# Kernel optimization log

Measured on AMD Instinct MI355X. Metric: run time of the kernel, lower is better.

The kernel has to match this reference:

```python
import jax, jax.numpy as jnp
import numpy as np

N, E, K = 20000, 320000, 4
IN, HID, OUT, HD = 512, 256, 128, 256


def setup_inputs() -> dict:
    key = jax.random.key(0)
    ks = jax.random.split(key, 12)
    def lin(k, fi, fo):
        return jax.random.normal(k, (fi, fo), jnp.float32) / np.sqrt(fi)
    return {
        "x": jax.random.normal(ks[0], (N, IN), jnp.float32),
        "edge_index": jax.random.randint(ks[1], (K, 2, E), 0, N),
        "value": jax.random.normal(ks[2], (K, 3), jnp.float32),
        "index": jax.random.randint(ks[3], (K, 2), 0, N),
        "W1": lin(ks[4], IN, HID),  "b1": jnp.zeros((HID,), jnp.float32),
        "W2": lin(ks[5], HID, OUT), "b2": jnp.zeros((OUT,), jnp.float32),
        "Wd": lin(ks[6], 2 * OUT + 3, HD), "bd": jnp.zeros((HD,), jnp.float32),
        "Wp": lin(ks[7], HD, 1),    "bp": jnp.zeros((1,), jnp.float32),
    }


def reference(x, edge_index, value, index, W1, b1, W2, b2, Wd, bd, Wp, bp):
    n = x.shape[0]
    loops = jnp.arange(n)

    def gcn(h, src, dst, W, b):
        # GCNConv: symmetric normalization with self-loops already in src/dst
        deg = jnp.zeros((n,), h.dtype).at[dst].add(1.0)
        dinv = jnp.where(deg > 0, deg ** -0.5, 0.0)
        norm = dinv[src] * dinv[dst]                      # [E+N]
        msg = (h @ W)[src] * norm[:, None]                # [E+N, F_out]
        return jnp.zeros((n, W.shape[1]), h.dtype).at[dst].add(msg) + b

    def encode(ei):
        src = jnp.concatenate([ei[0], loops])             # add self-loops
        dst = jnp.concatenate([ei[1], loops])
        h = jax.nn.relu(gcn(x, src, dst, W1, b1))
        return gcn(h, src, dst, W2, b2)                   # [N, OUT]

    def step(carry, inp):
        ei, val, idx = inp
        mu = encode(ei)
        h = jnp.concatenate([mu[idx[0]], mu[idx[1]], val])  # [2*OUT+3]
        o = jax.nn.relu(h @ Wd + bd)
        p = jax.nn.sigmoid(o @ Wp + bp)
        return carry, p[0]

    _, preds = jax.lax.scan(step, None, (edge_index, value, index))
    return preds  # [K]
```

## Files before the change

kernel.cpp:

```cpp
#include <hip/hip_runtime.h>
#include <hip/hip_bf16.h>

#define NN 20000
#define EE 320000
#define E4 (EE/4)
#define KK 4
#define FIN 512
#define FHID 256
#define FOUT 128
#define FHD 256
#define NH (2*FOUT+3)
#define CAP1 1024
#define MS2 128
#define BCAP 256

__device__ __forceinline__ float dinvf(int indeg) {
  return rsqrtf((float)(indeg + 1));
}

__global__ __launch_bounds__(256) void kz_zero(int4* __restrict__ p, int n4) {
  int i = blockIdx.x * 256 + threadIdx.x;
  if (i < n4) p[i] = make_int4(0, 0, 0, 0);
}

__global__ __launch_bounds__(256) void k12_scan_claim(const int* __restrict__ ei,
                                                      const int* __restrict__ idx,
                                                      int* __restrict__ cnt1,
                                                      int* __restrict__ L1src,
                                                      int* __restrict__ L1sel,
                                                      int* __restrict__ reg,
                                                      int* __restrict__ slotNode,
                                                      int* __restrict__ mslots) {
  int k = blockIdx.y;
  int* rk = reg + (size_t)k * NN;
  int t0 = idx[2 * k], t1 = idx[2 * k + 1];
  if (blockIdx.x == 0 && threadIdx.x < 2) {
    int node = (threadIdx.x == 0) ? t0 : t1;
    if (atomicCAS(&rk[node], 0, -2) == 0) {
      int s = atomicAdd(&mslots[k], 1);
      if (s < MS2) { slotNode[k * MS2 + s] = node; rk[node] = s + 1; }
    }
  }
  int e4 = blockIdx.x * blockDim.x + threadIdx.x;
  if (e4 >= E4) return;
  const int* srcp = ei + (size_t)k * 2 * EE;
  int4 d4 = ((const int4*)(srcp + EE))[e4];
  int ds[4] = {d4.x, d4.y, d4.z, d4.w};
  #pragma unroll
  for (int c = 0; c < 4; c++) {
    bool h0 = (ds[c] == t0), h1 = (ds[c] == t1);
    if (h0 || h1) {
      int u = srcp[e4 * 4 + c];
      if (h0) {
        int p = atomicAdd(&cnt1[k], 1);
        if (p < CAP1) { L1src[k * CAP1 + p] = u; L1sel[k * CAP1 + p] = 0; }
      }
      if (h1) {
        int p = atomicAdd(&cnt1[k], 1);
        if (p < CAP1) { L1src[k * CAP1 + p] = u; L1sel[k * CAP1 + p] = 1; }
      }
      if (atomicCAS(&rk[u], 0, -2) == 0) {
        int s = atomicAdd(&mslots[k], 1);
        if (s < MS2) { slotNode[k * MS2 + s] = u; rk[u] = s + 1; }
      }
    }
  }
}

__global__ __launch_bounds__(256) void k3_scanL2(const int* __restrict__ ei,
                                                 int* __restrict__ reg,
                                                 int* __restrict__ bcnt,
                                                 int* __restrict__ bucket) {
  int k = blockIdx.y;
  int e4 = blockIdx.x * blockDim.x + threadIdx.x;
  if (e4 >= E4) return;
  const int* srcp = ei + (size_t)k * 2 * EE;
  int4 d4 = ((const int4*)(srcp + EE))[e4];
  int* rk = reg + (size_t)k * NN;
  int ds[4] = {d4.x, d4.y, d4.z, d4.w};
  #pragma unroll
  for (int c = 0; c < 4; c++) {
    int rv = rk[ds[c]];
    if (rv > 0) {
      int s = rv - 1;
      int u = srcp[e4 * 4 + c];
      int p = atomicAdd(&bcnt[k * MS2 + s], 1);
      if (p < BCAP) bucket[((size_t)k * MS2 + s) * BCAP + p] = u;
      if (rk[u] == 0) rk[u] = -1;
    }
  }
}

__global__ __launch_bounds__(256) void k4_deg(const int* __restrict__ ei,
                                              const int* __restrict__ reg,
                                              int* __restrict__ deg) {
  int k = blockIdx.y;
  int e4 = blockIdx.x * blockDim.x + threadIdx.x;
  if (e4 >= E4) return;
  const int* dstp = ei + (size_t)k * 2 * EE + EE;
  int4 d4 = ((const int4*)dstp)[e4];
  const int* rk = reg + (size_t)k * NN;
  int ds[4] = {d4.x, d4.y, d4.z, d4.w};
  #pragma unroll
  for (int c = 0; c < 4; c++) {
    if (rk[ds[c]] != 0) atomicAdd(&deg[k * NN + ds[c]], 1);
  }
}

__global__ __launch_bounds__(1024) void k5_slotmlp(const int* __restrict__ slotNode,
                                                   const int* __restrict__ mslots,
                                                   const int* __restrict__ bcnt,
                                                   const int* __restrict__ bucket,
                                                   const int* __restrict__ deg,
                                                   const float* __restrict__ x,
                                                   const float* __restrict__ W1,
                                                   const float* __restrict__ b1,
                                                   const float* __restrict__ W2,
                                                   float* __restrict__ HW2) {
  __shared__ float aggS[FIN];
  __shared__ float gtmp[FIN];
  __shared__ float part[4][FHID];
  __shared__ float hrow[FHID];
  __shared__ float part2[8][FOUT];
  __shared__ int   uS[BCAP];
  __shared__ float duS[BCAP];
  int k = blockIdx.y, s = blockIdx.x;
  if (s >= mslots[k]) return;
  int tid = threadIdx.x;
  int node = slotNode[k * MS2 + s];
  int nb = min(bcnt[k * MS2 + s], BCAP);
  const int* bk = bucket + ((size_t)k * MS2 + s) * BCAP;
  for (int e = tid; e < nb; e += 1024) {
    int u = bk[e];
    uS[e] = u;
    duS[e] = dinvf(deg[k * NN + u]);
  }
  __syncthreads();
  float dn = dinvf(deg[k * NN + node]);
  int f = tid & (FIN - 1), half = tid >> 9;
  float a = (half == 0) ? dn * x[(size_t)node * FIN + f] : 0.f;
  for (int e = half; e < nb; e += 2) a += duS[e] * x[(size_t)uS[e] * FIN + f];
  if (half == 1) gtmp[f] = a;
  __syncthreads();
  if (half == 0) aggS[f] = dn * (a + gtmp[f]);
  __syncthreads();
  {
    int q = tid >> 8, j = tid & (FHID - 1);
    float acc = 0.f;
    const float* w1p = W1 + (size_t)(q * 128) * FHID + j;
    const float* ap = aggS + q * 128;
    #pragma unroll 8
    for (int kk = 0; kk < 128; kk++) acc += ap[kk] * w1p[(size_t)kk * FHID];
    part[q][j] = acc;
  }
  __syncthreads();
  if (tid < FHID) {
    float v = part[0][tid] + part[1][tid] + part[2][tid] + part[3][tid] + b1[tid];
    hrow[tid] = v > 0.f ? v : 0.f;
  }
  __syncthreads();
  {
    int p = tid >> 7, j = tid & (FOUT - 1);
    float a2 = 0.f;
    const float* w2p = W2 + (size_t)(p * 32) * FOUT + j;
    const float* hp = hrow + p * 32;
    #pragma unroll 8
    for (int kk = 0; kk < 32; kk++) a2 += hp[kk] * w2p[(size_t)kk * FOUT];
    part2[p][j] = a2;
  }
  __syncthreads();
  if (tid < FOUT) {
    float sv = part2[0][tid] + part2[1][tid] + part2[2][tid] + part2[3][tid] +
               part2[4][tid] + part2[5][tid] + part2[6][tid] + part2[7][tid];
    HW2[((size_t)k * MS2 + s) * FOUT + tid] = sv;
  }
}

__global__ __launch_bounds__(256) void k6_decode(const float* __restrict__ HW2,
                                                 const float* __restrict__ b2,
                                                 const int* __restrict__ cnt1,
                                                 const int* __restrict__ L1src,
                                                 const int* __restrict__ L1sel,
                                                 const int* __restrict__ idx,
                                                 const int* __restrict__ reg,
                                                 const int* __restrict__ deg,
                                                 const float* __restrict__ value,
                                                 const float* __restrict__ Wd,
                                                 const float* __restrict__ bd,
                                                 const float* __restrict__ Wp,
                                                 const float* __restrict__ bp,
                                                 float* __restrict__ out) {
  __shared__ float h[NH + 1];
  __shared__ float o[FHD];
  __shared__ float red[4];
  int k = blockIdx.x;
  int tid = threadIdx.x;
  const int* rk = reg + (size_t)k * NN;
  int n1 = min(cnt1[k], CAP1);
  int tsel = tid >> 7, j = tid & 127;
  int t = idx[2 * k + tsel];
  float dit = dinvf(deg[k * NN + t]);
  int tslot = rk[t] - 1;
  float acc = b2[j] + dit * dit * HW2[((size_t)k * MS2 + tslot) * FOUT + j];
  for (int i = 0; i < n1; i++) {
    if (L1sel[k * CAP1 + i] == tsel) {
      int s = L1src[k * CAP1 + i];
      float dis = dinvf(deg[k * NN + s]);
      int sslot = rk[s] - 1;
      acc += dis * dit * HW2[((size_t)k * MS2 + sslot) * FOUT + j];
    }
  }
  h[tsel * FOUT + j] = acc;
  if (tid < 3) h[2 * FOUT + tid] = value[k * 3 + tid];
  __syncthreads();
  float a2 = bd[tid];
  for (int i = 0; i < NH; i++) a2 += h[i] * Wd[(size_t)i * FHD + tid];
  o[tid] = a2 > 0.f ? a2 : 0.f;
  __syncthreads();
  float r = o[tid] * Wp[tid];
  for (int off2 = 32; off2 > 0; off2 >>= 1) r += __shfl_down(r, off2);
  if ((tid & 63) == 0) red[tid >> 6] = r;
  __syncthreads();
  if (tid == 0) {
    float ssum = red[0] + red[1] + red[2] + red[3] + bp[0];
    out[k] = 1.f / (1.f + expf(-ssum));
  }
}

extern "C" void kernel_launch(void* const* d_in, const int* in_sizes, int n_in,
                              void* d_out, int out_size, void* d_ws, size_t ws_size,
                              hipStream_t stream) {
  const float* x     = (const float*)d_in[0];
  const int*   ei    = (const int*)d_in[1];
  const float* value = (const float*)d_in[2];
  const int*   idx   = (const int*)d_in[3];
  const float* W1    = (const float*)d_in[4];
  const float* b1    = (const float*)d_in[5];
  const float* W2    = (const float*)d_in[6];
  const float* b2    = (const float*)d_in[7];
  const float* Wd    = (const float*)d_in[8];
  const float* bd    = (const float*)d_in[9];
  const float* Wp    = (const float*)d_in[10];
  const float* bp    = (const float*)d_in[11];
  float* out = (float*)d_out;

  char* ws = (char*)d_ws;
  size_t off = 0;
  auto alloc = [&](size_t bytes) -> void* {
    void* p = ws + off;
    off = (off + bytes + 255) & ~(size_t)255;
    return p;
  };
  int* reg   = (int*)alloc((size_t)(2 * KK * NN + KK * MS2 + 2 * KK) * sizeof(int));
  int* deg   = reg + KK * NN;
  int* bcnt  = deg + KK * NN;
  int* cnt1  = bcnt + KK * MS2;
  int* mslots = cnt1 + KK;
  size_t zbytes = (size_t)(2 * KK * NN + KK * MS2 + 2 * KK) * sizeof(int);
  int* L1src = (int*)alloc((size_t)KK * CAP1 * sizeof(int));
  int* L1sel = (int*)alloc((size_t)KK * CAP1 * sizeof(int));
  int* slotNode = (int*)alloc((size_t)KK * MS2 * sizeof(int));
  int* bucket = (int*)alloc((size_t)KK * MS2 * BCAP * sizeof(int));
  float* HW2 = (float*)alloc((size_t)KK * MS2 * FOUT * sizeof(float));
  (void)ws_size; (void)in_sizes; (void)n_in; (void)out_size;

  int n4 = (int)(zbytes / 16);
  kz_zero<<<(n4 + 255) / 256, 256, 0, stream>>>((int4*)reg, n4);

  dim3 escan((E4 + 255) / 256, KK);
  k12_scan_claim<<<escan, 256, 0, stream>>>(ei, idx, cnt1, L1src, L1sel,
                                            reg, slotNode, mslots);
  k3_scanL2<<<escan, 256, 0, stream>>>(ei, reg, bcnt, bucket);
  k4_deg<<<escan, 256, 0, stream>>>(ei, reg, deg);
  k5_slotmlp<<<dim3(MS2, KK), 1024, 0, stream>>>(slotNode, mslots, bcnt, bucket, deg,
                                                 x, W1, b1, W2, HW2);
  k6_decode<<<dim3(KK), 256, 0, stream>>>(HW2, b2, cnt1, L1src, L1sel, idx, reg, deg,
                                          value, Wd, bd, Wp, bp, out);
}
```

Before: 68.18 us.

## Fuse degree counting into first edge scan and unroll slot aggregation

Degree counting now runs inside the first edge scan as an unconditional atomic on every destination, so the separate k4_deg pass over all edges goes away and the dst array is read one time fewer. Both scan kernels switch to a fixed 160-block grid-stride loop, and the second scan no longer marks two-hop source nodes in the registry. The slot MLP neighbour aggregation is unrolled with four independent accumulators to expose more memory-level parallelism. In exchange, every edge now issues a global atomic rather than only edges into registered nodes, which adds atomic traffic.

```diff
diff --git a/kernel.cpp b/kernel.cpp
--- a/kernel.cpp
+++ b/kernel.cpp
@@ -13,6 +13,7 @@
 #define CAP1 1024
 #define MS2 128
 #define BCAP 256
+#define SCANB 160
 
 __device__ __forceinline__ float dinvf(int indeg) {
   return rsqrtf((float)(indeg + 1));
@@ -23,16 +24,18 @@
   if (i < n4) p[i] = make_int4(0, 0, 0, 0);
 }
 
-__global__ __launch_bounds__(256) void k12_scan_claim(const int* __restrict__ ei,
-                                                      const int* __restrict__ idx,
-                                                      int* __restrict__ cnt1,
-                                                      int* __restrict__ L1src,
-                                                      int* __restrict__ L1sel,
-                                                      int* __restrict__ reg,
-                                                      int* __restrict__ slotNode,
-                                                      int* __restrict__ mslots) {
+__global__ __launch_bounds__(256) void k12d_scan(const int* __restrict__ ei,
+                                                 const int* __restrict__ idx,
+                                                 int* __restrict__ cnt1,
+                                                 int* __restrict__ L1src,
+                                                 int* __restrict__ L1sel,
+                                                 int* __restrict__ reg,
+                                                 int* __restrict__ slotNode,
+                                                 int* __restrict__ mslots,
+                                                 int* __restrict__ deg) {
   int k = blockIdx.y;
   int* rk = reg + (size_t)k * NN;
+  int* dk = deg + k * NN;
   int t0 = idx[2 * k], t1 = idx[2 * k + 1];
   if (blockIdx.x == 0 && threadIdx.x < 2) {
     int node = (threadIdx.x == 0) ? t0 : t1;
@@ -41,69 +44,55 @@
       if (s < MS2) { slotNode[k * MS2 + s] = node; rk[node] = s + 1; }
     }
   }
-  int e4 = blockIdx.x * blockDim.x + threadIdx.x;
-  if (e4 >= E4) return;
   const int* srcp = ei + (size_t)k * 2 * EE;
-  int4 d4 = ((const int4*)(srcp + EE))[e4];
-  int ds[4] = {d4.x, d4.y, d4.z, d4.w};
-  #pragma unroll
-  for (int c = 0; c < 4; c++) {
-    bool h0 = (ds[c] == t0), h1 = (ds[c] == t1);
-    if (h0 || h1) {
-      int u = srcp[e4 * 4 + c];
-      if (h0) {
-        int p = atomicAdd(&cnt1[k], 1);
-        if (p < CAP1) { L1src[k * CAP1 + p] = u; L1sel[k * CAP1 + p] = 0; }
+  const int4* dst4 = (const int4*)(srcp + EE);
+  for (int e4 = blockIdx.x * 256 + threadIdx.x; e4 < E4; e4 += SCANB * 256) {
+    int4 d4 = dst4[e4];
+    int ds[4] = {d4.x, d4.y, d4.z, d4.w};
+    #pragma unroll
+    for (int c = 0; c < 4; c++) {
+      atomicAdd(dk + ds[c], 1);
+      bool h0 = (ds[c] == t0), h1 = (ds[c] == t1);
+      if (h0 || h1) {
+        int u = srcp[e4 * 4 + c];
+        if (h0) {
+          int p = atomicAdd(&cnt1[k], 1);
+          if (p < CAP1) { L1src[k * CAP1 + p] = u; L1sel[k * CAP1 + p] = 0; }
+        }
+        if (h1) {
+          int p = atomicAdd(&cnt1[k], 1);
+          if (p < CAP1) { L1src[k * CAP1 + p] = u; L1sel[k * CAP1 + p] = 1; }
+        }
+        if (atomicCAS(&rk[u], 0, -2) == 0) {
+          int s = atomicAdd(&mslots[k], 1);
+          if (s < MS2) { slotNode[k * MS2 + s] = u; rk[u] = s + 1; }
+        }
       }
-      if (h1) {
-        int p = atomicAdd(&cnt1[k], 1);
-        if (p < CAP1) { L1src[k * CAP1 + p] = u; L1sel[k * CAP1 + p] = 1; }
-      }
-      if (atomicCAS(&rk[u], 0, -2) == 0) {
-        int s = atomicAdd(&mslots[k], 1);
-        if (s < MS2) { slotNode[k * MS2 + s] = u; rk[u] = s + 1; }
-      }
     }
   }
 }
 
 __global__ __launch_bounds__(256) void k3_scanL2(const int* __restrict__ ei,
-                                                 int* __restrict__ reg,
+                                                 const int* __restrict__ reg,
                                                  int* __restrict__ bcnt,
                                                  int* __restrict__ bucket) {
   int k = blockIdx.y;
-  int e4 = blockIdx.x * blockDim.x + threadIdx.x;
-  if (e4 >= E4) return;
   const int* srcp = ei + (size_t)k * 2 * EE;
-  int4 d4 = ((const int4*)(srcp + EE))[e4];
-  int* rk = reg + (size_t)k * NN;
-  int ds[4] = {d4.x, d4.y, d4.z, d4.w};
-  #pragma unroll
-  for (int c = 0; c < 4; c++) {
-    int rv = rk[ds[c]];
-    if (rv > 0) {
-      int s = rv - 1;
-      int u = srcp[e4 * 4 + c];
-      int p = atomicAdd(&bcnt[k * MS2 + s], 1);
-      if (p < BCAP) bucket[((size_t)k * MS2 + s) * BCAP + p] = u;
-      if (rk[u] == 0) rk[u] = -1;
-    }
-  }
-}
-
-__global__ __launch_bounds__(256) void k4_deg(const int* __restrict__ ei,
-                                              const int* __restrict__ reg,
-                                              int* __restrict__ deg) {
-  int k = blockIdx.y;
-  int e4 = blockIdx.x * blockDim.x + threadIdx.x;
-  if (e4 >= E4) return;
-  const int* dstp = ei + (size_t)k * 2 * EE + EE;
-  int4 d4 = ((const int4*)dstp)[e4];
+  const int4* dst4 = (const int4*)(srcp + EE);
   const int* rk = reg + (size_t)k * NN;
-  int ds[4] = {d4.x, d4.y, d4.z, d4.w};
-  #pragma unroll
-  for (int c = 0; c < 4; c++) {
-    if (rk[ds[c]] != 0) atomicAdd(&deg[k * NN + ds[c]], 1);
+  for (int e4 = blockIdx.x * 256 + threadIdx.x; e4 < E4; e4 += SCANB * 256) {
+    int4 d4 = dst4[e4];
+    int ds[4] = {d4.x, d4.y, d4.z, d4.w};
+    #pragma unroll
+    for (int c = 0; c < 4; c++) {
+      int rv = rk[ds[c]];
+      if (rv > 0) {
+        int s = rv - 1;
+        int u = srcp[e4 * 4 + c];
+        int p = atomicAdd(&bcnt[k * MS2 + s], 1);
+        if (p < BCAP) bucket[((size_t)k * MS2 + s) * BCAP + p] = u;
+      }
+    }
   }
 }
 
@@ -138,8 +127,17 @@
   __syncthreads();
   float dn = dinvf(deg[k * NN + node]);
   int f = tid & (FIN - 1), half = tid >> 9;
-  float a = (half == 0) ? dn * x[(size_t)node * FIN + f] : 0.f;
-  for (int e = half; e < nb; e += 2) a += duS[e] * x[(size_t)uS[e] * FIN + f];
+  float a0 = (half == 0) ? dn * x[(size_t)node * FIN + f] : 0.f;
+  float a1 = 0.f, a2g = 0.f, a3 = 0.f;
+  int e = half;
+  for (; e + 6 < nb; e += 8) {
+    a0  += duS[e]     * x[(size_t)uS[e]     * FIN + f];
+    a1  += duS[e + 2] * x[(size_t)uS[e + 2] * FIN + f];
+    a2g += duS[e + 4] * x[(size_t)uS[e + 4] * FIN + f];
+    a3  += duS[e + 6] * x[(size_t)uS[e + 6] * FIN + f];
+  }
+  for (; e < nb; e += 2) a0 += duS[e] * x[(size_t)uS[e] * FIN + f];
+  float a = (a0 + a1) + (a2g + a3);
   if (half == 1) gtmp[f] = a;
   __syncthreads();
   if (half == 0) aggS[f] = dn * (a + gtmp[f]);
@@ -265,13 +263,12 @@
   (void)ws_size; (void)in_sizes; (void)n_in; (void)out_size;
 
   int n4 = (int)(zbytes / 16);
+  dim3 escan(SCANB, KK);
+
   kz_zero<<<(n4 + 255) / 256, 256, 0, stream>>>((int4*)reg, n4);
-
-  dim3 escan((E4 + 255) / 256, KK);
-  k12_scan_claim<<<escan, 256, 0, stream>>>(ei, idx, cnt1, L1src, L1sel,
-                                            reg, slotNode, mslots);
+  k12d_scan<<<escan, 256, 0, stream>>>(ei, idx, cnt1, L1src, L1sel,
+                                       reg, slotNode, mslots, deg);
   k3_scanL2<<<escan, 256, 0, stream>>>(ei, reg, bcnt, bucket);
-  k4_deg<<<escan, 256, 0, stream>>>(ei, reg, deg);
   k5_slotmlp<<<dim3(MS2, KK), 1024, 0, stream>>>(slotNode, mslots, bcnt, bucket, deg,
                                                  x, W1, b1, W2, HW2);
   k6_decode<<<dim3(KK), 256, 0, stream>>>(HW2, b2, cnt1, L1src, L1sel, idx, reg, deg,
```

Result: slower. 109.0 us (+59.9%).
